# Kernel optimization log

Hardware: AMD Instinct MI355X
Metric: run time of the kernel (lower is better)

## Reference

```python
import jax, jax.numpy as jnp
import numpy as np

B, T, D = 8, 4096, 1024
H, HD = 8, 128            # head_dim = ceil(D/H)
P = H * HD                # proj_dim = 1024
OUT = 1024
WIN, STRIDE = 64, 32


def _window_index(seq_len, win, stride):
    # mirrors the Python start-list construction in RollingAttentionPooling.forward
    starts = list(range(0, max(1, seq_len), stride))
    if starts and starts[-1] + win < seq_len:
        starts.append(seq_len - win)
    starts = sorted(set(max(0, s) for s in starts))
    idx = np.asarray(starts)[:, None] + np.arange(win)[None, :]
    valid = idx < seq_len
    idx = np.minimum(idx, seq_len - 1)
    return jnp.asarray(idx, dtype=jnp.int32), jnp.asarray(valid)


def setup_inputs() -> dict:
    key = jax.random.key(0)
    k0, k1, k2, k3 = jax.random.split(key, 4)
    x = jax.random.normal(k0, (B, T, D), dtype=jnp.float32)
    w_kv = jax.random.normal(k1, (D, 2 * P), dtype=jnp.float32) * 0.02
    query = jax.random.normal(k2, (H, HD), dtype=jnp.float32)
    w_out_w = jax.random.normal(k3, (OUT, P), dtype=jnp.float32) * 0.02
    w_out_b = jnp.zeros((OUT,), dtype=jnp.float32)
    return {"x": x, "w_kv": w_kv, "query": query, "w_out_w": w_out_w, "w_out_b": w_out_b}


def reference(x, w_kv, query, w_out_w, w_out_b):
    bsz, seq_len, _ = x.shape
    # K/V projection computed once for the whole sequence (same math as
    # recomputing per-window, since windows are slices of x).
    kv = (x @ w_kv).reshape(bsz, seq_len, 2, H, HD)
    k = kv[:, :, 0]                                   # (B, T, H, HD)
    v = kv[:, :, 1]                                   # (B, T, H, HD)
    logits = jnp.einsum('bthd,hd->bht', k, query) / jnp.sqrt(jnp.float32(HD))

    idx, valid = _window_index(seq_len, WIN, STRIDE)
    lw = logits[:, :, idx]
    lw = jnp.where(valid[None, None], lw, -jnp.inf)
    scores = jax.nn.softmax(lw.astype(jnp.float32), axis=-1).astype(v.dtype)
    vw = v[:, idx]
    pooled = jnp.einsum('bhwt,bwthd->bwhd', scores, vw)
    pooled = pooled.reshape(bsz, idx.shape[0], P)     # (B, W, P)
    out_w = pooled @ w_out_w.T + w_out_b              # (B, W, OUT)
    return out_w.mean(axis=1)                         # (B, OUT)
```

## Files before the change

### kernel.cpp

```cpp
#include <hip/hip_runtime.h>

#define B_ 8
#define T_ 4096
#define D_ 1024
#define H_ 8
#define HD_ 128
#define P_ 1024
#define OUT_ 1024
#define W_ 128
#define NPC_ 64
#define PCH_ 16

#define TRL_ 32
#define DKL_ 128
#define NKC_ (D_ / DKL_)
#define LSTR_ (DKL_ + 4)

__global__ void __launch_bounds__(256) k_qproj(const float* __restrict__ w_kv,
                                               const float* __restrict__ query,
                                               float* __restrict__ qp) {
  int d = blockIdx.x;
  int t = threadIdx.x;
  float4 wv = ((const float4*)(w_kv + (size_t)d * (2 * P_)))[t];
  float4 qv = ((const float4*)query)[t];
  float a = wv.x * qv.x + wv.y * qv.y + wv.z * qv.z + wv.w * qv.w;
#pragma unroll
  for (int off = 16; off; off >>= 1) a += __shfl_xor(a, off, 64);
  if ((t & 31) == 0) {
    int h = t >> 5;
    qp[h * D_ + d] = a * 0.08838834764831845f;
  }
}

__global__ void __launch_bounds__(256) k_logits(const float* __restrict__ x,
                                                const float* __restrict__ qp,
                                                float* __restrict__ logits) {
  __shared__ float s_x[TRL_ * LSTR_];
  __shared__ float s_q[H_ * LSTR_];
  const int t = threadIdx.x;
  const int r = t >> 3;
  const int h = t & 7;
  const int R0 = blockIdx.x * TRL_;
  const int b = R0 >> 12, t0 = R0 & (T_ - 1);

  const float4* xg = (const float4*)x;
  const float4* qg = (const float4*)qp;

  float4 stx[4];
  float4 stq;
#pragma unroll
  for (int q = 0; q < 4; ++q) {
    int i = t + 256 * q;
    int row = i >> 5, c4 = i & 31;
    stx[q] = xg[((size_t)(R0 + row) << 8) + c4];
  }
  {
    int hh = t >> 5, c4 = t & 31;
    stq = qg[(hh << 8) + c4];
  }

  float4 a4 = make_float4(0.f, 0.f, 0.f, 0.f);
  for (int kc = 0; kc < NKC_; ++kc) {
    __syncthreads();
#pragma unroll
    for (int q = 0; q < 4; ++q) {
      int i = t + 256 * q;
      int row = i >> 5, c4 = i & 31;
      *(float4*)&s_x[row * LSTR_ + 4 * c4] = stx[q];
    }
    {
      int hh = t >> 5, c4 = t & 31;
      *(float4*)&s_q[hh * LSTR_ + 4 * c4] = stq;
    }
    __syncthreads();
    if (kc + 1 < NKC_) {
      int kb = (kc + 1) << 5;
#pragma unroll
      for (int q = 0; q < 4; ++q) {
        int i = t + 256 * q;
        int row = i >> 5, c4 = i & 31;
        stx[q] = xg[((size_t)(R0 + row) << 8) + kb + c4];
      }
      int hh = t >> 5, c4 = t & 31;
      stq = qg[(hh << 8) + kb + c4];
    }
#pragma unroll
    for (int k4 = 0; k4 < DKL_ / 4; ++k4) {
      float4 xv = *(const float4*)&s_x[r * LSTR_ + 4 * k4];
      float4 qv = *(const float4*)&s_q[h * LSTR_ + 4 * k4];
      a4.x += xv.x * qv.x; a4.y += xv.y * qv.y;
      a4.z += xv.z * qv.z; a4.w += xv.w * qv.w;
    }
  }
  float acc = (a4.x + a4.y) + (a4.z + a4.w);
  logits[((b * H_ + h) << 12) + t0 + r] = acc;
}

__global__ void __launch_bounds__(256) k_yacc(const float* __restrict__ x,
                                              const float* __restrict__ logits,
                                              float* __restrict__ partial,
                                              int chunk) {
  int c = blockIdx.x;
  int b = blockIdx.y;
  int t0 = c * chunk;
  int W0 = (t0 >> 5) - 1;
  int nwl = (chunk >> 5) + 1;
  __shared__ float sw[H_][64];
  __shared__ float sm[4][H_], srs[4][H_];
  int tid = threadIdx.x;
  if (tid < nwl * H_) {
    int wi = tid >> 3, h = tid & 7;
    int w = W0 + wi;
    if (w >= 0 && w < W_) {
      const float* L = logits + (((size_t)(b * H_ + h)) << 12) + (w << 5);
      int cnt = min(64, T_ - (w << 5));
      float m = -1e30f;
#pragma unroll 8
      for (int i = 0; i < cnt; ++i) m = fmaxf(m, L[i]);
      float s = 0.f;
#pragma unroll 8
      for (int i = 0; i < cnt; ++i) s += __expf(L[i] - m);
      sm[wi][h] = m;
      srs[wi][h] = 1.0f / s;
    }
  }
  __syncthreads();
  const float invW = 1.0f / (float)W_;
  for (int i = tid; i < H_ * chunk; i += 256) {
    int h = i / chunk, tt = i - h * chunk;
    int tg = t0 + tt;
    float l = logits[(((size_t)(b * H_ + h)) << 12) + tg];
    int w1 = tg >> 5;
    int rel = w1 - W0;
    float acc = __expf(l - sm[rel][h]) * srs[rel][h];
    if (w1 > 0) acc += __expf(l - sm[rel - 1][h]) * srs[rel - 1][h];
    sw[h][tt] = acc * invW;
  }
  __syncthreads();
  float4 acc[H_];
#pragma unroll
  for (int h = 0; h < H_; ++h) acc[h] = make_float4(0.f, 0.f, 0.f, 0.f);
  const float4* xb = (const float4*)(x + ((size_t)b * T_ + t0) * D_);
#pragma unroll 4
  for (int tt = 0; tt < chunk; ++tt) {
    float4 xv = xb[tt * (D_ / 4) + threadIdx.x];
#pragma unroll
    for (int h = 0; h < H_; ++h) {
      float wv = sw[h][tt];
      acc[h].x += wv * xv.x; acc[h].y += wv * xv.y;
      acc[h].z += wv * xv.z; acc[h].w += wv * xv.w;
    }
  }
  float4* pp = (float4*)(partial + (((size_t)(c * B_ + b) * H_) << 10));
#pragma unroll
  for (int h = 0; h < H_; ++h) pp[h * (D_ / 4) + threadIdx.x] = acc[h];
}

__global__ void __launch_bounds__(256) k_reduce_y(const float* __restrict__ partial,
                                                  float* __restrict__ y, int nc) {
  int i = blockIdx.x * blockDim.x + threadIdx.x;
  float4 a = make_float4(0.f, 0.f, 0.f, 0.f);
  const float4* p = (const float4*)partial;
#pragma unroll 8
  for (int c = 0; c < nc; ++c) {
    float4 v = p[(size_t)c * (B_ * H_ * D_ / 4) + i];
    a.x += v.x; a.y += v.y; a.z += v.z; a.w += v.w;
  }
  ((float4*)y)[i] = a;
}

__global__ void __launch_bounds__(256) k_pooled_part(const float* __restrict__ y,
                                                     const float* __restrict__ w_kv,
                                                     float* __restrict__ ppart) {
  int c = blockIdx.x;
  int d0 = c * PCH_;
  int t = threadIdx.x;
  int h = t >> 5;
  __shared__ float sy[PCH_][B_ * H_];
  for (int i = t; i < PCH_ * B_ * H_; i += 256) {
    int dd = i >> 6, bh = i & 63;
    sy[dd][bh] = y[((size_t)bh << 10) + d0 + dd];
  }
  __syncthreads();
  float4 acc[B_];
#pragma unroll
  for (int b = 0; b < B_; ++b) acc[b] = make_float4(0.f, 0.f, 0.f, 0.f);
#pragma unroll
  for (int dd = 0; dd < PCH_; ++dd) {
    float4 wv = ((const float4*)(w_kv + (size_t)(d0 + dd) * (2 * P_) + P_))[t];
#pragma unroll
    for (int b = 0; b < B_; ++b) {
      float yv = sy[dd][b * H_ + h];
      acc[b].x += yv * wv.x; acc[b].y += yv * wv.y;
      acc[b].z += yv * wv.z; acc[b].w += yv * wv.w;
    }
  }
#pragma unroll
  for (int b = 0; b < B_; ++b)
    ((float4*)(ppart + (((size_t)c * B_ + b) << 10)))[t] = acc[b];
}

__global__ void __launch_bounds__(256) k_reduce_pooled(const float* __restrict__ ppart,
                                                       float* __restrict__ pooled) {
  int i = blockIdx.x * 256 + threadIdx.x;
  int b = i >> 8, p4 = i & 255;
  float4 a = make_float4(0.f, 0.f, 0.f, 0.f);
  const float4* p = (const float4*)ppart;
#pragma unroll 8
  for (int c = 0; c < NPC_; ++c) {
    float4 v = p[((c * B_ + b) << 8) + p4];
    a.x += v.x; a.y += v.y; a.z += v.z; a.w += v.w;
  }
  ((float4*)pooled)[i] = a;
}

__global__ void __launch_bounds__(256) k_out(const float* __restrict__ pooled,
                                             const float* __restrict__ w_out_w,
                                             const float* __restrict__ w_out_b,
                                             float* __restrict__ out) {
  int wid = threadIdx.x >> 6, lane = threadIdx.x & 63;
  int o = blockIdx.x * 4 + wid;
  const float4* wr = (const float4*)(w_out_w + (size_t)o * P_);
  float4 wv[4];
#pragma unroll
  for (int j = 0; j < 4; ++j) wv[j] = wr[lane + 64 * j];
  float res[B_];
#pragma unroll
  for (int b = 0; b < B_; ++b) {
    const float4* pb = (const float4*)(pooled + b * P_);
    float a = 0.f;
#pragma unroll
    for (int j = 0; j < 4; ++j) {
      float4 pv = pb[lane + 64 * j];
      a += wv[j].x * pv.x + wv[j].y * pv.y + wv[j].z * pv.z + wv[j].w * pv.w;
    }
#pragma unroll
    for (int off = 32; off; off >>= 1) a += __shfl_down(a, off, 64);
    res[b] = a;
  }
  if (lane == 0) {
    float bias = w_out_b[o];
#pragma unroll
    for (int b = 0; b < B_; ++b) out[b * OUT_ + o] = res[b] + bias;
  }
}

extern "C" void kernel_launch(void* const* d_in, const int* in_sizes, int n_in,
                              void* d_out, int out_size, void* d_ws, size_t ws_size,
                              hipStream_t stream) {
  const float* x       = (const float*)d_in[0];
  const float* w_kv    = (const float*)d_in[1];
  const float* query   = (const float*)d_in[2];
  const float* w_out_w = (const float*)d_in[3];
  const float* w_out_b = (const float*)d_in[4];
  float* out = (float*)d_out;

  size_t need128 = ((size_t)8192 + 262144 + (size_t)128 * B_ * H_ * D_ + 65536 + 8192) * 4;
  int nc = (ws_size >= need128) ? 128 : 64;
  int chunk = T_ / nc;

  float* ws = (float*)d_ws;
  float* qp      = ws;
  float* logits  = qp + H_ * D_;
  float* partial = logits + B_ * H_ * T_;
  float* y       = partial + (size_t)nc * B_ * H_ * D_;
  float* pooled  = y + B_ * H_ * D_;
  float* ppart   = partial;

  k_qproj<<<D_, 256, 0, stream>>>(w_kv, query, qp);
  k_logits<<<B_ * T_ / TRL_, 256, 0, stream>>>(x, qp, logits);
  k_yacc<<<dim3(nc, B_), 256, 0, stream>>>(x, logits, partial, chunk);
  k_reduce_y<<<(B_ * H_ * D_ / 4) / 256, 256, 0, stream>>>(partial, y, nc);
  k_pooled_part<<<NPC_, 256, 0, stream>>>(y, w_kv, ppart);
  k_reduce_pooled<<<(B_ * P_ / 4) / 256, 256, 0, stream>>>(ppart, pooled);
  k_out<<<OUT_ / 4, 256, 0, stream>>>(pooled, w_out_w, w_out_b, out);
}
```

Before: 295.4 us.

## Enlarge logits row tile with LDS-staged coalesced stores; batch x loads in yacc

The logits kernel now handles 64 rows per block instead of 32. Each thread computes two rows, so every q vector loaded from shared memory is reused twice, and results are staged through shared memory so the logits writes are coalesced. The yacc kernel transposes its window-weight table to [t][h], which lets it fetch all 8 head weights with two float4 reads. It also issues 8 row loads of x ahead of the FMAs to raise memory-level parallelism. These changes add register pressure (8 staged float4s plus accumulators) and halve the number of logits blocks.

Measured after the change: 277.1 us. 1.07x faster.

```diff
diff --git a/kernel.cpp b/kernel.cpp
--- a/kernel.cpp
+++ b/kernel.cpp
@@ -11,7 +11,7 @@
 #define NPC_ 64
 #define PCH_ 16
 
-#define TRL_ 32
+#define TRL_ 64
 #define DKL_ 128
 #define NKC_ (D_ / DKL_)
 #define LSTR_ (DKL_ + 4)
@@ -37,6 +37,7 @@
                                                 float* __restrict__ logits) {
   __shared__ float s_x[TRL_ * LSTR_];
   __shared__ float s_q[H_ * LSTR_];
+  __shared__ float s_out[H_][TRL_];
   const int t = threadIdx.x;
   const int r = t >> 3;
   const int h = t & 7;
@@ -46,10 +47,10 @@
   const float4* xg = (const float4*)x;
   const float4* qg = (const float4*)qp;
 
-  float4 stx[4];
+  float4 stx[8];
   float4 stq;
 #pragma unroll
-  for (int q = 0; q < 4; ++q) {
+  for (int q = 0; q < 8; ++q) {
     int i = t + 256 * q;
     int row = i >> 5, c4 = i & 31;
     stx[q] = xg[((size_t)(R0 + row) << 8) + c4];
@@ -59,11 +60,12 @@
     stq = qg[(hh << 8) + c4];
   }
 
-  float4 a4 = make_float4(0.f, 0.f, 0.f, 0.f);
+  float4 a0 = make_float4(0.f, 0.f, 0.f, 0.f);
+  float4 a1 = make_float4(0.f, 0.f, 0.f, 0.f);
   for (int kc = 0; kc < NKC_; ++kc) {
     __syncthreads();
 #pragma unroll
-    for (int q = 0; q < 4; ++q) {
+    for (int q = 0; q < 8; ++q) {
       int i = t + 256 * q;
       int row = i >> 5, c4 = i & 31;
       *(float4*)&s_x[row * LSTR_ + 4 * c4] = stx[q];
@@ -76,7 +78,7 @@
     if (kc + 1 < NKC_) {
       int kb = (kc + 1) << 5;
 #pragma unroll
-      for (int q = 0; q < 4; ++q) {
+      for (int q = 0; q < 8; ++q) {
         int i = t + 256 * q;
         int row = i >> 5, c4 = i & 31;
         stx[q] = xg[((size_t)(R0 + row) << 8) + kb + c4];
@@ -86,14 +88,21 @@
     }
 #pragma unroll
     for (int k4 = 0; k4 < DKL_ / 4; ++k4) {
-      float4 xv = *(const float4*)&s_x[r * LSTR_ + 4 * k4];
       float4 qv = *(const float4*)&s_q[h * LSTR_ + 4 * k4];
-      a4.x += xv.x * qv.x; a4.y += xv.y * qv.y;
-      a4.z += xv.z * qv.z; a4.w += xv.w * qv.w;
-    }
-  }
-  float acc = (a4.x + a4.y) + (a4.z + a4.w);
-  logits[((b * H_ + h) << 12) + t0 + r] = acc;
+      float4 x0 = *(const float4*)&s_x[r * LSTR_ + 4 * k4];
+      float4 x1 = *(const float4*)&s_x[(r + 32) * LSTR_ + 4 * k4];
+      a0.x += x0.x * qv.x; a0.y += x0.y * qv.y; a0.z += x0.z * qv.z; a0.w += x0.w * qv.w;
+      a1.x += x1.x * qv.x; a1.y += x1.y * qv.y; a1.z += x1.z * qv.z; a1.w += x1.w * qv.w;
+    }
+  }
+  s_out[h][r]      = (a0.x + a0.y) + (a0.z + a0.w);
+  s_out[h][r + 32] = (a1.x + a1.y) + (a1.z + a1.w);
+  __syncthreads();
+  {
+    int hh = t >> 5, j = t & 31;
+    float2 val = *(const float2*)&s_out[hh][2 * j];
+    *(float2*)&logits[(((size_t)(b * H_ + hh)) << 12) + t0 + 2 * j] = val;
+  }
 }
 
 __global__ void __launch_bounds__(256) k_yacc(const float* __restrict__ x,
@@ -105,7 +114,7 @@
   int t0 = c * chunk;
   int W0 = (t0 >> 5) - 1;
   int nwl = (chunk >> 5) + 1;
-  __shared__ float sw[H_][64];
+  __shared__ float sw[64][H_];
   __shared__ float sm[4][H_], srs[4][H_];
   int tid = threadIdx.x;
   if (tid < nwl * H_) {
@@ -134,26 +143,34 @@
     int rel = w1 - W0;
     float acc = __expf(l - sm[rel][h]) * srs[rel][h];
     if (w1 > 0) acc += __expf(l - sm[rel - 1][h]) * srs[rel - 1][h];
-    sw[h][tt] = acc * invW;
+    sw[tt][h] = acc * invW;
   }
   __syncthreads();
   float4 acc[H_];
 #pragma unroll
   for (int h = 0; h < H_; ++h) acc[h] = make_float4(0.f, 0.f, 0.f, 0.f);
   const float4* xb = (const float4*)(x + ((size_t)b * T_ + t0) * D_);
-#pragma unroll 4
-  for (int tt = 0; tt < chunk; ++tt) {
-    float4 xv = xb[tt * (D_ / 4) + threadIdx.x];
-#pragma unroll
-    for (int h = 0; h < H_; ++h) {
-      float wv = sw[h][tt];
-      acc[h].x += wv * xv.x; acc[h].y += wv * xv.y;
-      acc[h].z += wv * xv.z; acc[h].w += wv * xv.w;
+  for (int tt0 = 0; tt0 < chunk; tt0 += 8) {
+    float4 xv[8];
+#pragma unroll
+    for (int j = 0; j < 8; ++j) xv[j] = xb[(tt0 + j) * (D_ / 4) + tid];
+#pragma unroll
+    for (int j = 0; j < 8; ++j) {
+      float4 wa = *(const float4*)&sw[tt0 + j][0];
+      float4 wb = *(const float4*)&sw[tt0 + j][4];
+      acc[0].x += wa.x * xv[j].x; acc[0].y += wa.x * xv[j].y; acc[0].z += wa.x * xv[j].z; acc[0].w += wa.x * xv[j].w;
+      acc[1].x += wa.y * xv[j].x; acc[1].y += wa.y * xv[j].y; acc[1].z += wa.y * xv[j].z; acc[1].w += wa.y * xv[j].w;
+      acc[2].x += wa.z * xv[j].x; acc[2].y += wa.z * xv[j].y; acc[2].z += wa.z * xv[j].z; acc[2].w += wa.z * xv[j].w;
+      acc[3].x += wa.w * xv[j].x; acc[3].y += wa.w * xv[j].y; acc[3].z += wa.w * xv[j].z; acc[3].w += wa.w * xv[j].w;
+      acc[4].x += wb.x * xv[j].x; acc[4].y += wb.x * xv[j].y; acc[4].z += wb.x * xv[j].z; acc[4].w += wb.x * xv[j].w;
+      acc[5].x += wb.y * xv[j].x; acc[5].y += wb.y * xv[j].y; acc[5].z += wb.y * xv[j].z; acc[5].w += wb.y * xv[j].w;
+      acc[6].x += wb.z * xv[j].x; acc[6].y += wb.z * xv[j].y; acc[6].z += wb.z * xv[j].z; acc[6].w += wb.z * xv[j].w;
+      acc[7].x += wb.w * xv[j].x; acc[7].y += wb.w * xv[j].y; acc[7].z += wb.w * xv[j].z; acc[7].w += wb.w * xv[j].w;
     }
   }
   float4* pp = (float4*)(partial + (((size_t)(c * B_ + b) * H_) << 10));
 #pragma unroll
-  for (int h = 0; h < H_; ++h) pp[h * (D_ / 4) + threadIdx.x] = acc[h];
+  for (int h = 0; h < H_; ++h) pp[h * (D_ / 4) + tid] = acc[h];
 }
 
 __global__ void __launch_bounds__(256) k_reduce_y(const float* __restrict__ partial,
```
